# Performance work log

Hardware: AMD Instinct MI355X
Metric: run time of the kernel (lower is better)

Reference implementation:

```python
import jax, jax.numpy as jnp
import numpy as np
import math

B, T, C, H = 2, 2048, 1024, 16
HD = C // H  # head_dim = 64


def setup_inputs() -> dict:
    key = jax.random.key(0)
    ks = jax.random.split(key, 10)
    s = 1.0 / math.sqrt(C)
    x = jax.random.normal(ks[0], (B, T, C), jnp.float32)
    wq = jax.random.normal(ks[1], (C, C), jnp.float32) * s
    wk = jax.random.normal(ks[2], (C, C), jnp.float32) * s
    wv = jax.random.normal(ks[3], (C, C), jnp.float32) * s
    wo = jax.random.normal(ks[4], (C, C), jnp.float32) * s
    bq = jnp.zeros((C,), jnp.float32)
    bk = jnp.zeros((C,), jnp.float32)
    bv = jnp.zeros((C,), jnp.float32)
    bo = jnp.zeros((C,), jnp.float32)
    fractal_dim = jnp.ones((1,), jnp.float32)  # scalar fractal dimension input
    alpha = jnp.asarray(1.5, jnp.float32)
    fractal_alpha_scale = jnp.asarray(0.5, jnp.float32)
    energy_normalizer = jnp.asarray(1.0, jnp.float32)
    return {"x": x, "fractal_dim": fractal_dim, "wq": wq, "bq": bq, "wk": wk,
            "bk": bk, "wv": wv, "bv": bv, "wo": wo, "bo": bo, "alpha": alpha,
            "fractal_alpha_scale": fractal_alpha_scale,
            "energy_normalizer": energy_normalizer}


def reference(x, fractal_dim, wq, bq, wk, bk, wv, bv, wo, bo, alpha,
              fractal_alpha_scale, energy_normalizer):
    b, t, c = x.shape
    # input energy: L2 norm over channels, [b, t, 1]
    input_energy = jnp.linalg.norm(x, axis=-1, keepdims=True)
    adaptive_alpha = alpha + fractal_alpha_scale * (fractal_dim - 1.5)  # [1]

    q = (x @ wq + bq).reshape(b, t, H, HD)
    k = (x @ wk + bk).reshape(b, t, H, HD)
    v = (x @ wv + bv).reshape(b, t, H, HD)

    # per-head FFT along the time axis -> complex64
    q_fft = jnp.fft.fft(q, axis=1)
    k_fft = jnp.fft.fft(k, axis=1)
    v_fft = jnp.fft.fft(v, axis=1)

    freqs = jnp.fft.fftfreq(t).astype(jnp.float32)  # [t]
    phase = adaptive_alpha * jnp.arctan(jnp.log(jnp.abs(freqs) + 1e-10))  # [t]
    # unit-modulus complex spectral filter, broadcast [1, t, 1, 1]
    filt = jax.lax.complex(jnp.cos(phase), jnp.sin(phase))[None, :, None, None]

    qf = q_fft * filt
    kf = k_fft * filt
    vf = v_fft * filt

    # real part of complex matmul Q_f @ K_f^T, computed without complex GEMM:
    # Re(qf kf^T) = qr kr^T - qi ki^T
    inv_sqrt = np.float32(1.0 / math.sqrt(HD))
    logits = (jnp.einsum('bthd,bshd->bhts', qf.real, kf.real)
              - jnp.einsum('bthd,bshd->bhts', qf.imag, kf.imag)) * inv_sqrt
    attn = jax.nn.softmax(logits, axis=-1)  # [b, h, t, s]

    # attn is real, so Re(attn @ vf) = attn @ Re(vf); out_proj has real weights
    # so taking the real part before the projection is exact.
    attended = jnp.einsum('bhts,bshd->bthd', attn, vf.real)
    out = attended.reshape(b, t, c) @ wo + bo

    out_energy = jnp.linalg.norm(out, axis=-1, keepdims=True)
    energy_ratio = input_energy / (out_energy + 1e-8)
    return out * energy_ratio * energy_normalizer
```

## Files before the change

### kernel.cpp

```cpp
#include <hip/hip_runtime.h>
#include <math.h>


typedef _Float16 half8 __attribute__((ext_vector_type(8)));
typedef _Float16 half4 __attribute__((ext_vector_type(4)));
typedef float f32x4 __attribute__((ext_vector_type(4)));
#define MFMA16 __builtin_amdgcn_mfma_f32_16x16x32_f16

#define GLOAD16(g, l) __builtin_amdgcn_global_load_lds( \
    (const __attribute__((address_space(1))) void*)(g), \
    (__attribute__((address_space(3))) void*)(l), 16, 0, 0)

__device__ inline void split2(float v, _Float16& h, _Float16& l) {
    h = (_Float16)v;
    l = (_Float16)((v - (float)h) * 2048.0f);
}
__device__ inline unsigned pack_split(float v) {
    _Float16 h, l;
    split2(v, h, l);
    union { _Float16 f; unsigned short u; } a, b;
    a.f = h; b.f = l;
    return (unsigned)a.u | ((unsigned)b.u << 16);
}
__device__ inline _Float16 lo16(unsigned u) {
    union { unsigned short s; _Float16 f; } x; x.s = (unsigned short)(u & 0xffffu); return x.f;
}
__device__ inline _Float16 hi16(unsigned u) {
    union { unsigned short s; _Float16 f; } x; x.s = (unsigned short)(u >> 16); return x.f;
}
__device__ inline float2 cmul(float2 a, float2 b) {
    return make_float2(a.x * b.x - a.y * b.y, a.x * b.y + a.y * b.x);
}

__device__ inline void write_split(_Float16* dh, _Float16* dl, uint4 u0, uint4 u1) {
    uint4 lo, hi;
    lo.x = __builtin_amdgcn_perm(u0.y, u0.x, 0x05040100u);
    lo.y = __builtin_amdgcn_perm(u0.w, u0.z, 0x05040100u);
    lo.z = __builtin_amdgcn_perm(u1.y, u1.x, 0x05040100u);
    lo.w = __builtin_amdgcn_perm(u1.w, u1.z, 0x05040100u);
    hi.x = __builtin_amdgcn_perm(u0.y, u0.x, 0x07060302u);
    hi.y = __builtin_amdgcn_perm(u0.w, u0.z, 0x07060302u);
    hi.z = __builtin_amdgcn_perm(u1.y, u1.x, 0x07060302u);
    hi.w = __builtin_amdgcn_perm(u1.w, u1.z, 0x07060302u);
    *(uint4*)dh = lo;
    *(uint4*)dl = hi;
}

__global__ __launch_bounds__(256) void k_init_tables(
    float2* __restrict__ tw, float2* __restrict__ filt,
    const float* __restrict__ fd, const float* __restrict__ alpha,
    const float* __restrict__ fas)
{
    int i = blockIdx.x * 256 + threadIdx.x;
    double aa = (double)alpha[0] + (double)fas[0] * ((double)fd[0] - 1.5);
    if (i < 1024) {
        double ang = -2.0 * 3.14159265358979323846 * (double)i / 2048.0;
        double s, c;
        sincos(ang, &s, &c);
        tw[i] = make_float2((float)c, (float)s);
    }
    if (i < 2048) {
        double fr = (i < 1024) ? (double)i / 2048.0 : ((double)i - 2048.0) / 2048.0;
        double ph = aa * atan(log(fabs(fr) + 1e-10));
        double s, c;
        sincos(ph, &s, &c);
        filt[i] = make_float2((float)c, (float)s);
    }
}

__global__ __launch_bounds__(256) void k_prep_wpl3(
    const float* __restrict__ wq, const float* __restrict__ wk,
    const float* __restrict__ wv, _Float16* __restrict__ wpl)
{
    __shared__ float tile[64][65];
    const int z = blockIdx.z;
    const float* W = (z == 0) ? wq : (z == 1) ? wk : wv;
    _Float16* Whi = wpl + (size_t)z * 2097152;
    _Float16* Wlo = Whi + 1048576;
    const int kb = blockIdx.x * 64, cb = blockIdx.y * 64;
    const int t = threadIdx.x, r = t >> 4, c4 = (t & 15) * 4;
#pragma unroll
    for (int i = 0; i < 4; ++i) {
        int row = r + 16 * i;
        float4 v = *(const float4*)&W[(size_t)(kb + row) * 1024 + cb + c4];
        tile[row][c4 + 0] = v.x; tile[row][c4 + 1] = v.y;
        tile[row][c4 + 2] = v.z; tile[row][c4 + 3] = v.w;
    }
    __syncthreads();
#pragma unroll
    for (int h = 0; h < 2; ++h) {
        int idx = t + h * 256;
        int lane = idx & 63, kt2 = (idx >> 6) & 1, ct = idx >> 7;
        int cl = ct * 16 + (lane & 15);
        int kl = kt2 * 32 + ((lane >> 4) * 8);
        half8 hv, lv;
#pragma unroll
        for (int j = 0; j < 8; ++j) {
            _Float16 hh, ll;
            split2(tile[kl + j][cl], hh, ll);
            hv[j] = hh; lv[j] = ll;
        }
        size_t u = ((size_t)((cb >> 4) + ct) * 32 + (kb >> 5) + kt2) * 64 + lane;
        *(half8*)&Whi[u * 8] = hv;
        *(half8*)&Wlo[u * 8] = lv;
    }
}

__global__ __launch_bounds__(256) void k_prep_wpl1(
    const float* __restrict__ W, _Float16* __restrict__ wpl)
{
    __shared__ float tile[64][65];
    _Float16* Whi = wpl;
    _Float16* Wlo = wpl + 1048576;
    const int kb = blockIdx.x * 64, cb = blockIdx.y * 64;
    const int t = threadIdx.x, r = t >> 4, c4 = (t & 15) * 4;
#pragma unroll
    for (int i = 0; i < 4; ++i) {
        int row = r + 16 * i;
        float4 v = *(const float4*)&W[(size_t)(kb + row) * 1024 + cb + c4];
        tile[row][c4 + 0] = v.x; tile[row][c4 + 1] = v.y;
        tile[row][c4 + 2] = v.z; tile[row][c4 + 3] = v.w;
    }
    __syncthreads();
#pragma unroll
    for (int h = 0; h < 2; ++h) {
        int idx = t + h * 256;
        int lane = idx & 63, kt2 = (idx >> 6) & 1, ct = idx >> 7;
        int cl = ct * 16 + (lane & 15);
        int kl = kt2 * 32 + ((lane >> 4) * 8);
        half8 hv, lv;
#pragma unroll
        for (int j = 0; j < 8; ++j) {
            _Float16 hh, ll;
            split2(tile[kl + j][cl], hh, ll);
            hv[j] = hh; lv[j] = ll;
        }
        size_t u = ((size_t)((cb >> 4) + ct) * 32 + (kb >> 5) + kt2) * 64 + lane;
        *(half8*)&Whi[u * 8] = hv;
        *(half8*)&Wlo[u * 8] = lv;
    }
}

__global__ __launch_bounds__(256) void k_prep_xpl(
    const float* __restrict__ x, _Float16* __restrict__ xpl)
{
    __shared__ float tile[64][65];
    _Float16* Xhi = xpl;
    _Float16* Xlo = xpl + 4194304;
    const int nb = blockIdx.x * 64, cb = blockIdx.y * 64;
    const int t = threadIdx.x, r = t >> 4, c4 = (t & 15) * 4;
#pragma unroll
    for (int i = 0; i < 4; ++i) {
        int row = r + 16 * i;
        float4 v = *(const float4*)&x[(size_t)(nb + row) * 1024 + cb + c4];
        tile[row][c4 + 0] = v.x; tile[row][c4 + 1] = v.y;
        tile[row][c4 + 2] = v.z; tile[row][c4 + 3] = v.w;
    }
    __syncthreads();
#pragma unroll
    for (int h = 0; h < 2; ++h) {
        int idx = t + h * 256;
        int lane = idx & 63, ct2 = (idx >> 6) & 1, ntl = (idx >> 7) & 3;
        int nl = ntl * 16 + (lane & 15);
        int cl = ct2 * 32 + ((lane >> 4) * 8);
        half8 hv, lv;
#pragma unroll
        for (int j = 0; j < 8; ++j) {
            _Float16 hh, ll;
            split2(tile[nl][cl + j], hh, ll);
            hv[j] = hh; lv[j] = ll;
        }
        size_t u = ((size_t)((nb >> 4) + ntl) * 32 + (cb >> 5) + ct2) * 64 + lane;
        *(half8*)&Xhi[u * 8] = hv;
        *(half8*)&Xlo[u * 8] = lv;
    }
}

__global__ __launch_bounds__(256) void k_gemm_qkv(
    const _Float16* __restrict__ xpl, const _Float16* __restrict__ wpl,
    const float* __restrict__ bq, const float* __restrict__ bk,
    const float* __restrict__ bv,
    float* __restrict__ qT, float* __restrict__ kT, float* __restrict__ vT)
{
    __shared__ __align__(16) _Float16 Ab[2][8][2][64][8];
    __shared__ __align__(16) _Float16 Bb[2][8][2][64][8];
    const int tid = threadIdx.x;
    const int mat = blockIdx.z;
    const _Float16* Ahi = wpl + (size_t)mat * 2097152;
    const _Float16* Alo = Ahi + 1048576;
    const _Float16* Bhi = xpl;
    const _Float16* Blo = xpl + 4194304;
    const float* bias = (mat == 0) ? bq : (mat == 1) ? bk : bv;
    float* outp       = (mat == 0) ? qT : (mat == 1) ? kT : vT;
    const int m0 = blockIdx.x * 128, n0 = blockIdx.y * 128;
    const int w = tid >> 6, lane = tid & 63, quad = lane >> 4, l15 = lane & 15;
    const int wm = (w & 1) * 4, wn = (w >> 1) * 4;

    const int s0 = 2 * w, s1 = 2 * w + 1;
    const size_t aT0 = (size_t)((m0 >> 4) + s0) * 32;
    const size_t aT1 = aT0 + 32;
    const size_t bT0 = (size_t)((n0 >> 4) + s0) * 32;
    const size_t bT1 = bT0 + 32;
    const int ln8 = lane * 8;

    f32x4 acc1[4][4], acc2[4][4];
    const f32x4 z4 = {0.f, 0.f, 0.f, 0.f};
#pragma unroll
    for (int i = 0; i < 4; ++i)
#pragma unroll
        for (int j = 0; j < 4; ++j) { acc1[i][j] = z4; acc2[i][j] = z4; }

    {
        size_t oA0 = aT0 * 512 + ln8;
        size_t oA1 = aT1 * 512 + ln8;
        size_t oB0 = bT0 * 512 + ln8;
        size_t oB1 = bT1 * 512 + ln8;
        GLOAD16(Ahi + oA0, &Ab[0][s0][0][0][0]);
        GLOAD16(Alo + oA0, &Ab[0][s0][1][0][0]);
        GLOAD16(Ahi + oA1, &Ab[0][s1][0][0][0]);
        GLOAD16(Alo + oA1, &Ab[0][s1][1][0][0]);
        GLOAD16(Bhi + oB0, &Bb[0][s0][0][0][0]);
        GLOAD16(Blo + oB0, &Bb[0][s0][1][0][0]);
        GLOAD16(Bhi + oB1, &Bb[0][s1][0][0][0]);
        GLOAD16(Blo + oB1, &Bb[0][s1][1][0][0]);
    }
    __syncthreads();

    for (int kt = 0; kt < 32; ++kt) {
        const int cur = kt & 1, nxt = cur ^ 1;
        if (kt < 31) {
            int kn = kt + 1;
            size_t oA0 = (aT0 + kn) * 512 + ln8;
            size_t oA1 = (aT1 + kn) * 512 + ln8;
            size_t oB0 = (bT0 + kn) * 512 + ln8;
            size_t oB1 = (bT1 + kn) * 512 + ln8;
            GLOAD16(Ahi + oA0, &Ab[nxt][s0][0][0][0]);
            GLOAD16(Alo + oA0, &Ab[nxt][s0][1][0][0]);
            GLOAD16(Ahi + oA1, &Ab[nxt][s1][0][0][0]);
            GLOAD16(Alo + oA1, &Ab[nxt][s1][1][0][0]);
            GLOAD16(Bhi + oB0, &Bb[nxt][s0][0][0][0]);
            GLOAD16(Blo + oB0, &Bb[nxt][s0][1][0][0]);
            GLOAD16(Bhi + oB1, &Bb[nxt][s1][0][0][0]);
            GLOAD16(Blo + oB1, &Bb[nxt][s1][1][0][0]);
        }
        half8 ah[4], al[4];
#pragma unroll
        for (int mt = 0; mt < 4; ++mt) {
            ah[mt] = *(half8*)&Ab[cur][wm + mt][0][lane][0];
            al[mt] = *(half8*)&Ab[cur][wm + mt][1][lane][0];
        }
#pragma unroll
        for (int nt = 0; nt < 4; ++nt) {
            half8 bh = *(half8*)&Bb[cur][wn + nt][0][lane][0];
            half8 bl = *(half8*)&Bb[cur][wn + nt][1][lane][0];
#pragma unroll
            for (int mt = 0; mt < 4; ++mt) {
                acc1[mt][nt] = MFMA16(ah[mt], bh, acc1[mt][nt], 0, 0, 0);
                acc2[mt][nt] = MFMA16(ah[mt], bl, acc2[mt][nt], 0, 0, 0);
                acc2[mt][nt] = MFMA16(al[mt], bh, acc2[mt][nt], 0, 0, 0);
            }
        }
        __syncthreads();
    }
    const int b_ = n0 >> 11, t0 = n0 & 2047;
#pragma unroll
    for (int mt = 0; mt < 4; ++mt) {
#pragma unroll
        for (int r_ = 0; r_ < 4; ++r_) {
            int m = m0 + (wm + mt) * 16 + quad * 4 + r_;
            float bs = bias[m];
            float* orow = &outp[(size_t)(b_ * 1024 + m) * 2048 + t0];
#pragma unroll
            for (int nt = 0; nt < 4; ++nt) {
                float val = acc1[mt][nt][r_] + acc2[mt][nt][r_] * (1.f / 2048.f) + bs;
                orow[(wn + nt) * 16 + l15] = val;
            }
        }
    }
}

#define SFI(i) ((i) + ((i) >> 4))
__global__ __launch_bounds__(256) void k_fft_filter(
    float* __restrict__ qT, float* __restrict__ kT, float* __restrict__ vT,
    float* __restrict__ qiT, float* __restrict__ kiT,
    const float2* __restrict__ tw, const float2* __restrict__ filt)
{
    __shared__ float2 sf[2176];
    const int bid = blockIdx.x;
    const int mat = bid >> 10;
    const int pair = bid & 1023;
    const int seq0 = pair * 2, seq1 = seq0 + 1;
    float* base = (mat == 0) ? qT : (mat == 1) ? kT : vT;
    float* src0 = base + (size_t)seq0 * 2048;
    float* src1 = base + (size_t)seq1 * 2048;
    const int tid = threadIdx.x;

    for (int i = tid; i < 2048; i += 256) {
        int j = (int)(__brev((unsigned)i) >> 21);
        sf[SFI(j)] = make_float2(src0[i], src1[i]);
    }
    __syncthreads();
#pragma unroll
    for (int st = 1; st <= 9; st += 2) {
        const int h = 1 << (st - 1);
        const int s = 11 - st;
        for (int u = tid; u < 512; u += 256) {
            int m = u & (h - 1);
            int g = u >> (st - 1);
            int bi = g * 4 * h + m;
            float2 a = sf[SFI(bi)], b = sf[SFI(bi + h)];
            float2 c = sf[SFI(bi + 2 * h)], d = sf[SFI(bi + 3 * h)];
            float2 W  = tw[m << s];
            float2 W2 = tw[m << (s - 1)];
            float2 wb = cmul(W, b), wd = cmul(W, d);
            float2 a1 = make_float2(a.x + wb.x, a.y + wb.y);
            float2 b1 = make_float2(a.x - wb.x, a.y - wb.y);
            float2 c1 = make_float2(c.x + wd.x, c.y + wd.y);
            float2 d1 = make_float2(c.x - wd.x, c.y - wd.y);
            float2 w2c = cmul(W2, c1);
            float2 w2d = cmul(W2, d1);
            float2 w3d = make_float2(w2d.y, -w2d.x);
            sf[SFI(bi)]         = make_float2(a1.x + w2c.x, a1.y + w2c.y);
            sf[SFI(bi + 2 * h)] = make_float2(a1.x - w2c.x, a1.y - w2c.y);
            sf[SFI(bi + h)]     = make_float2(b1.x + w3d.x, b1.y + w3d.y);
            sf[SFI(bi + 3 * h)] = make_float2(b1.x - w3d.x, b1.y - w3d.y);
        }
        __syncthreads();
    }
    for (int u = tid; u < 1024; u += 256) {
        float2 w = tw[u];
        float2 a = sf[SFI(u)], b = sf[SFI(u + 1024)];
        float2 wb = cmul(w, b);
        sf[SFI(u)]        = make_float2(a.x + wb.x, a.y + wb.y);
        sf[SFI(u + 1024)] = make_float2(a.x - wb.x, a.y - wb.y);
    }
    __syncthreads();

    unsigned* dr0 = (unsigned*)src0;
    unsigned* dr1 = (unsigned*)src1;
    unsigned* di0 = (mat == 0) ? (unsigned*)(qiT + (size_t)seq0 * 2048)
                               : (unsigned*)(kiT + (size_t)seq0 * 2048);
    unsigned* di1 = (mat == 0) ? (unsigned*)(qiT + (size_t)seq1 * 2048)
                               : (unsigned*)(kiT + (size_t)seq1 * 2048);
    for (int i = tid; i < 2048; i += 256) {
        float2 z  = sf[SFI(i)];
        float2 zm = sf[SFI((2048 - i) & 2047)];
        float Are = 0.5f * (z.x + zm.x), Aim = 0.5f * (z.y - zm.y);
        float Bre = 0.5f * (z.y + zm.y), Bim = 0.5f * (zm.x - z.x);
        float2 f = filt[i];
        float re0 = Are * f.x - Aim * f.y, im0 = Are * f.y + Aim * f.x;
        float re1 = Bre * f.x - Bim * f.y, im1 = Bre * f.y + Bim * f.x;
        if (mat == 0) {
            dr0[i] = pack_split(0.125f * re0); di0[i] = pack_split(0.125f * im0);
            dr1[i] = pack_split(0.125f * re1); di1[i] = pack_split(0.125f * im1);
        } else if (mat == 1) {
            dr0[i] = pack_split(re0); di0[i] = pack_split(-im0);
            dr1[i] = pack_split(re1); di1[i] = pack_split(-im1);
        } else {
            dr0[i] = pack_split(re0);
            dr1[i] = pack_split(re1);
        }
    }
}

__global__ __launch_bounds__(512, 2) void k_flash(
    const unsigned* __restrict__ qpk, const unsigned* __restrict__ qipk,
    const unsigned* __restrict__ kpk, const unsigned* __restrict__ kipk,
    const unsigned* __restrict__ vpk, _Float16* __restrict__ attpl)
{
    __shared__ __align__(16) _Float16 Kbuf[2][4][4][2][64][8];
    __shared__ __align__(16) _Float16 Vbuf[2][2][4][2][64][8];

    const int tid = threadIdx.x;
    const int w = tid >> 6, lane = tid & 63;
    const int quad = lane >> 4, l15 = lane & 15;
    const int p = blockIdx.x;
    const int bh = (p & 7) * 4 + (p >> 6);
    const int tb = (p >> 3) & 7;
    const size_t bc = (size_t)bh * 64;
    const int tw0 = tb * 256 + w * 16;

    half8 aqh[2][4], aql[2][4];
#pragma unroll
    for (int rg = 0; rg < 2; ++rg) {
#pragma unroll
        for (int kc = 0; kc < 4; ++kc) {
#pragma unroll
            for (int j = 0; j < 8; ++j) {
                int d = kc * 32 + quad * 8 + j;
                int t = tw0 + rg * 128 + l15;
                unsigned u = (d < 64) ? qpk[(bc + d) * 2048 + t]
                                      : qipk[(bc + d - 64) * 2048 + t];
                aqh[rg][kc][j] = lo16(u);
                aql[rg][kc][j] = hi16(u);
            }
        }
    }

    f32x4 O1[2][4], O2[2][4];
    const f32x4 zero4 = {0.f, 0.f, 0.f, 0.f};
#pragma unroll
    for (int rg = 0; rg < 2; ++rg)
#pragma unroll
        for (int nt = 0; nt < 4; ++nt) { O1[rg][nt] = zero4; O2[rg][nt] = zero4; }
    float m_[2] = {-3e38f, -3e38f};
    float l_[2] = {0.f, 0.f};

    const int sK = tid & 63;
    const int dc0 = tid >> 6;
    const int stK = sK >> 4;
    const int kcK0 = dc0 >> 2;
    const int laneK = (sK & 15) + ((dc0 & 3) << 4);
    const unsigned* kre = &kpk[(bc + dc0 * 8) * 2048 + sK];
    const unsigned* kim = &kipk[(bc + dc0 * 8) * 2048 + sK];
    const int sc2V = tid >> 8;
    const int ntV = (tid >> 6) & 3, laneV = tid & 63;
    const int dV = ntV * 16 + (laneV & 15);
    const int s0V = sc2V * 32 + (laneV >> 4) * 4;
    const unsigned* vbase = &vpk[(bc + dV) * 2048 + s0V];

    unsigned ka0, ka1, ka2, ka3, ka4, ka5, ka6, ka7;
    unsigned kb0, kb1, kb2, kb3, kb4, kb5, kb6, kb7;
    uint4 va0, va1;
    ka0 = kre[0 * 2048]; ka1 = kre[1 * 2048];
    ka2 = kre[2 * 2048]; ka3 = kre[3 * 2048];
    ka4 = kre[4 * 2048]; ka5 = kre[5 * 2048];
    ka6 = kre[6 * 2048]; ka7 = kre[7 * 2048];
    kb0 = kim[0 * 2048]; kb1 = kim[1 * 2048];
    kb2 = kim[2 * 2048]; kb3 = kim[3 * 2048];
    kb4 = kim[4 * 2048]; kb5 = kim[5 * 2048];
    kb6 = kim[6 * 2048]; kb7 = kim[7 * 2048];
    va0 = *(const uint4*)vbase;
    va1 = *(const uint4*)(vbase + 16);
    write_split(&Kbuf[0][stK][kcK0][0][laneK][0], &Kbuf[0][stK][kcK0][1][laneK][0],
                make_uint4(ka0, ka1, ka2, ka3), make_uint4(ka4, ka5, ka6, ka7));
    write_split(&Kbuf[0][stK][kcK0 + 2][0][laneK][0], &Kbuf[0][stK][kcK0 + 2][1][laneK][0],
                make_uint4(kb0, kb1, kb2, kb3), make_uint4(kb4, kb5, kb6, kb7));
    write_split(&Vbuf[0][sc2V][ntV][0][laneV][0], &Vbuf[0][sc2V][ntV][1][laneV][0],
                va0, va1);
    kre += 64; kim += 64; vbase += 64;
    ka0 = kre[0 * 2048]; ka1 = kre[1 * 2048];
    ka2 = kre[2 * 2048]; ka3 = kre[3 * 2048];
    ka4 = kre[4 * 2048]; ka5 = kre[5 * 2048];
    ka6 = kre[6 * 2048]; ka7 = kre[7 * 2048];
    kb0 = kim[0 * 2048]; kb1 = kim[1 * 2048];
    kb2 = kim[2 * 2048]; kb3 = kim[3 * 2048];
    kb4 = kim[4 * 2048]; kb5 = kim[5 * 2048];
    kb6 = kim[6 * 2048]; kb7 = kim[7 * 2048];
    va0 = *(const uint4*)vbase;
    va1 = *(const uint4*)(vbase + 16);
    __syncthreads();

    for (int it = 0; it < 32; ++it) {
        const int cur = it & 1, nxt = cur ^ 1;
        if (it < 31) {
            write_split(&Kbuf[nxt][stK][kcK0][0][laneK][0],
                        &Kbuf[nxt][stK][kcK0][1][laneK][0],
                        make_uint4(ka0, ka1, ka2, ka3), make_uint4(ka4, ka5, ka6, ka7));
            write_split(&Kbuf[nxt][stK][kcK0 + 2][0][laneK][0],
                        &Kbuf[nxt][stK][kcK0 + 2][1][laneK][0],
                        make_uint4(kb0, kb1, kb2, kb3), make_uint4(kb4, kb5, kb6, kb7));
            write_split(&Vbuf[nxt][sc2V][ntV][0][laneV][0],
                        &Vbuf[nxt][sc2V][ntV][1][laneV][0], va0, va1);
        }
        if (it < 30) {
            kre += 64; kim += 64; vbase += 64;
            ka0 = kre[0 * 2048]; ka1 = kre[1 * 2048];
            ka2 = kre[2 * 2048]; ka3 = kre[3 * 2048];
            ka4 = kre[4 * 2048]; ka5 = kre[5 * 2048];
            ka6 = kre[6 * 2048]; ka7 = kre[7 * 2048];
            kb0 = kim[0 * 2048]; kb1 = kim[1 * 2048];
            kb2 = kim[2 * 2048]; kb3 = kim[3 * 2048];
            kb4 = kim[4 * 2048]; kb5 = kim[5 * 2048];
            kb6 = kim[6 * 2048]; kb7 = kim[7 * 2048];
            va0 = *(const uint4*)vbase;
            va1 = *(const uint4*)(vbase + 16);
        }

        f32x4 S1[2][4], S2[2][4];
#pragma unroll
        for (int rg = 0; rg < 2; ++rg)
#pragma unroll
            for (int st = 0; st < 4; ++st) { S1[rg][st] = zero4; S2[rg][st] = zero4; }
        __builtin_amdgcn_s_setprio(1);
#pragma unroll
        for (int st = 0; st < 4; ++st) {
#pragma unroll
            for (int kc = 0; kc < 4; ++kc) {
                half8 khf = *(half8*)&Kbuf[cur][st][kc][0][lane][0];
                half8 klf = *(half8*)&Kbuf[cur][st][kc][1][lane][0];
#pragma unroll
                for (int rg = 0; rg < 2; ++rg) {
                    S1[rg][st] = MFMA16(khf, aqh[rg][kc], S1[rg][st], 0, 0, 0);
                    S2[rg][st] = MFMA16(klf, aqh[rg][kc], S2[rg][st], 0, 0, 0);
                    S2[rg][st] = MFMA16(khf, aql[rg][kc], S2[rg][st], 0, 0, 0);
                }
            }
        }
        __builtin_amdgcn_s_setprio(0);

        half8 pb[2][2];
#pragma unroll
        for (int rg = 0; rg < 2; ++rg) {
#pragma unroll
            for (int st = 0; st < 4; ++st)
                S1[rg][st] = S1[rg][st] + S2[rg][st] * (1.f / 2048.f);
            float mt = -3e38f;
#pragma unroll
            for (int st = 0; st < 4; ++st)
#pragma unroll
                for (int r = 0; r < 4; ++r)
                    mt = fmaxf(mt, S1[rg][st][r]);
            mt = fmaxf(mt, __shfl_xor(mt, 16));
            mt = fmaxf(mt, __shfl_xor(mt, 32));
            if (!__all(mt <= m_[rg] + 8.f)) {
                float mn2 = fmaxf(m_[rg], mt);
                float al = __expf(m_[rg] - mn2);
                m_[rg] = mn2;
                l_[rg] *= al;
#pragma unroll
                for (int nt = 0; nt < 4; ++nt) { O1[rg][nt] *= al; O2[rg][nt] *= al; }
            }
            float mn = m_[rg];
            float rs = 0.f;
            _Float16 ph[4][4];
#pragma unroll
            for (int st = 0; st < 4; ++st)
#pragma unroll
                for (int r = 0; r < 4; ++r) {
                    float pe = __expf(S1[rg][st][r] - mn);
                    rs += pe;
                    ph[st][r] = (_Float16)pe;
                }
            rs += __shfl_xor(rs, 16);
            rs += __shfl_xor(rs, 32);
            l_[rg] += rs;
#pragma unroll
            for (int sc2 = 0; sc2 < 2; ++sc2) {
                half8 t8;
                t8[0] = ph[2 * sc2][0];     t8[1] = ph[2 * sc2][1];
                t8[2] = ph[2 * sc2][2];     t8[3] = ph[2 * sc2][3];
                t8[4] = ph[2 * sc2 + 1][0]; t8[5] = ph[2 * sc2 + 1][1];
                t8[6] = ph[2 * sc2 + 1][2]; t8[7] = ph[2 * sc2 + 1][3];
                pb[rg][sc2] = t8;
            }
        }

        __builtin_amdgcn_s_setprio(1);
#pragma unroll
        for (int sc2 = 0; sc2 < 2; ++sc2) {
#pragma unroll
            for (int nt = 0; nt < 4; ++nt) {
                half8 vh = *(half8*)&Vbuf[cur][sc2][nt][0][lane][0];
                half8 vl = *(half8*)&Vbuf[cur][sc2][nt][1][lane][0];
                O1[0][nt] = MFMA16(vh, pb[0][sc2], O1[0][nt], 0, 0, 0);
                O2[0][nt] = MFMA16(vl, pb[0][sc2], O2[0][nt], 0, 0, 0);
                O1[1][nt] = MFMA16(vh, pb[1][sc2], O1[1][nt], 0, 0, 0);
                O2[1][nt] = MFMA16(vl, pb[1][sc2], O2[1][nt], 0, 0, 0);
            }
        }
        __builtin_amdgcn_s_setprio(0);

        __syncthreads();
    }

    const int b = bh >> 4, h = bh & 15;
#pragma unroll
    for (int rg = 0; rg < 2; ++rg) {
        float inv = 1.0f / l_[rg];
        int mrow = b * 2048 + tw0 + rg * 128 + l15;
        size_t mt32 = (size_t)(mrow >> 4) * 32;
#pragma unroll
        for (int nt = 0; nt < 4; ++nt) {
            size_t u = (mt32 + h * 2 + (nt >> 1)) * 512
                     + (size_t)(l15 + 16 * ((nt * 2 + (quad >> 1)) & 3)) * 8
                     + (quad & 1) * 4;
            half4 hv, lv;
#pragma unroll
            for (int r = 0; r < 4; ++r) {
                float val = (O1[rg][nt][r] + O2[rg][nt][r] * (1.f / 2048.f)) * inv;
                _Float16 hh, ll;
                split2(val, hh, ll);
                hv[r] = hh; lv[r] = ll;
            }
            *(half4*)&attpl[u] = hv;
            *(half4*)&attpl[4194304 + u] = lv;
        }
    }
}

__global__ __launch_bounds__(256) void k_gemm_out(
    const _Float16* __restrict__ attpl, const _Float16* __restrict__ wopl,
    const float* __restrict__ bo, float* __restrict__ out)
{
    __shared__ __align__(16) _Float16 Ab[2][8][2][64][8];
    __shared__ __align__(16) _Float16 Bb[2][8][2][64][8];
    const int tid = threadIdx.x;
    const _Float16* Ahi = attpl;
    const _Float16* Alo = attpl + 4194304;
    const _Float16* Bhi = wopl;
    const _Float16* Blo = wopl + 1048576;
    const int m0 = blockIdx.x * 128, n0 = blockIdx.y * 128;
    const int w = tid >> 6, lane = tid & 63, quad = lane >> 4, l15 = lane & 15;
    const int wm = (w & 1) * 4, wn = (w >> 1) * 4;

    const int s0 = 2 * w, s1 = 2 * w + 1;
    const size_t aT0 = (size_t)((m0 >> 4) + s0) * 32;
    const size_t aT1 = aT0 + 32;
    const size_t bT0 = (size_t)((n0 >> 4) + s0) * 32;
    const size_t bT1 = bT0 + 32;
    const int ln8 = lane * 8;

    f32x4 acc1[4][4], acc2[4][4];
    const f32x4 z4 = {0.f, 0.f, 0.f, 0.f};
#pragma unroll
    for (int i = 0; i < 4; ++i)
#pragma unroll
        for (int j = 0; j < 4; ++j) { acc1[i][j] = z4; acc2[i][j] = z4; }

    {
        size_t oA0 = aT0 * 512 + ln8;
        size_t oA1 = aT1 * 512 + ln8;
        size_t oB0 = bT0 * 512 + ln8;
        size_t oB1 = bT1 * 512 + ln8;
        GLOAD16(Ahi + oA0, &Ab[0][s0][0][0][0]);
        GLOAD16(Alo + oA0, &Ab[0][s0][1][0][0]);
        GLOAD16(Ahi + oA1, &Ab[0][s1][0][0][0]);
        GLOAD16(Alo + oA1, &Ab[0][s1][1][0][0]);
        GLOAD16(Bhi + oB0, &Bb[0][s0][0][0][0]);
        GLOAD16(Blo + oB0, &Bb[0][s0][1][0][0]);
        GLOAD16(Bhi + oB1, &Bb[0][s1][0][0][0]);
        GLOAD16(Blo + oB1, &Bb[0][s1][1][0][0]);
    }
    __syncthreads();

    for (int kt = 0; kt < 32; ++kt) {
        const int cur = kt & 1, nxt = cur ^ 1;
        if (kt < 31) {
            int kn = kt + 1;
            size_t oA0 = (aT0 + kn) * 512 + ln8;
            size_t oA1 = (aT1 + kn) * 512 + ln8;
            size_t oB0 = (bT0 + kn) * 512 + ln8;
            size_t oB1 = (bT1 + kn) * 512 + ln8;
            GLOAD16(Ahi + oA0, &Ab[nxt][s0][0][0][0]);
            GLOAD16(Alo + oA0, &Ab[nxt][s0][1][0][0]);
            GLOAD16(Ahi + oA1, &Ab[nxt][s1][0][0][0]);
            GLOAD16(Alo + oA1, &Ab[nxt][s1][1][0][0]);
            GLOAD16(Bhi + oB0, &Bb[nxt][s0][0][0][0]);
            GLOAD16(Blo + oB0, &Bb[nxt][s0][1][0][0]);
            GLOAD16(Bhi + oB1, &Bb[nxt][s1][0][0][0]);
            GLOAD16(Blo + oB1, &Bb[nxt][s1][1][0][0]);
        }
        half8 ah[4], al[4];
#pragma unroll
        for (int mt = 0; mt < 4; ++mt) {
            ah[mt] = *(half8*)&Ab[cur][wm + mt][0][lane][0];
            al[mt] = *(half8*)&Ab[cur][wm + mt][1][lane][0];
        }
#pragma unroll
        for (int nt = 0; nt < 4; ++nt) {
            half8 bh = *(half8*)&Bb[cur][wn + nt][0][lane][0];
            half8 bl = *(half8*)&Bb[cur][wn + nt][1][lane][0];
#pragma unroll
            for (int mt = 0; mt < 4; ++mt) {
                acc1[mt][nt] = MFMA16(ah[mt], bh, acc1[mt][nt], 0, 0, 0);
                acc2[mt][nt] = MFMA16(ah[mt], bl, acc2[mt][nt], 0, 0, 0);
                acc2[mt][nt] = MFMA16(al[mt], bh, acc2[mt][nt], 0, 0, 0);
            }
        }
        __syncthreads();
    }
#pragma unroll
    for (int mt = 0; mt < 4; ++mt) {
#pragma unroll
        for (int r_ = 0; r_ < 4; ++r_) {
            int m = m0 + (wm + mt) * 16 + quad * 4 + r_;
            float* orow = &out[(size_t)m * 1024 + n0];
#pragma unroll
            for (int nt = 0; nt < 4; ++nt) {
                int n = (wn + nt) * 16 + l15;
                float val = acc1[mt][nt][r_] + acc2[mt][nt][r_] * (1.f / 2048.f)
                          + bo[n0 + n];
                orow[n] = val;
            }
        }
    }
}

__global__ __launch_bounds__(256) void k_norm(
    const float* __restrict__ x, float* __restrict__ out,
    const float* __restrict__ en)
{
    const int row = blockIdx.x;
    const int tid = threadIdx.x;
    const float* xr = x + (size_t)row * 1024;
    float* orow = out + (size_t)row * 1024;
    float4 xv = *(const float4*)&xr[tid * 4];
    float4 ov = *(const float4*)&orow[tid * 4];
    float ssx = xv.x * xv.x + xv.y * xv.y + xv.z * xv.z + xv.w * xv.w;
    float sso = ov.x * ov.x + ov.y * ov.y + ov.z * ov.z + ov.w * ov.w;
#pragma unroll
    for (int m = 1; m <= 32; m <<= 1) {
        ssx += __shfl_xor(ssx, m, 64);
        sso += __shfl_xor(sso, m, 64);
    }
    __shared__ float rx[4], ro[4];
    const int wid = tid >> 6;
    if ((tid & 63) == 0) { rx[wid] = ssx; ro[wid] = sso; }
    __syncthreads();
    float tsx = rx[0] + rx[1] + rx[2] + rx[3];
    float tso = ro[0] + ro[1] + ro[2] + ro[3];
    float scale = sqrtf(tsx) / (sqrtf(tso) + 1e-8f) * en[0];
    ov.x *= scale; ov.y *= scale; ov.z *= scale; ov.w *= scale;
    *(float4*)&orow[tid * 4] = ov;
}

extern "C" void kernel_launch(void* const* d_in, const int* in_sizes, int n_in,
                              void* d_out, int out_size, void* d_ws, size_t ws_size,
                              hipStream_t stream)
{
    const float* x     = (const float*)d_in[0];
    const float* fd    = (const float*)d_in[1];
    const float* wq    = (const float*)d_in[2];
    const float* bq    = (const float*)d_in[3];
    const float* wk    = (const float*)d_in[4];
    const float* bk    = (const float*)d_in[5];
    const float* wv    = (const float*)d_in[6];
    const float* bv    = (const float*)d_in[7];
    const float* wo    = (const float*)d_in[8];
    const float* bo    = (const float*)d_in[9];
    const float* alpha = (const float*)d_in[10];
    const float* fas   = (const float*)d_in[11];
    const float* en    = (const float*)d_in[12];
    float* out = (float*)d_out;
    float* ws  = (float*)d_ws;

    float* qT  = ws;
    float* kT  = ws + (size_t)1 * 4194304;
    float* vT  = ws + (size_t)2 * 4194304;
    float* qiT = ws + (size_t)3 * 4194304;
    float* kiT = ws + (size_t)4 * 4194304;
    float* att = ws + (size_t)5 * 4194304;
    float2* tw   = (float2*)(ws + (size_t)6 * 4194304);
    float2* filt = (float2*)(ws + (size_t)6 * 4194304 + 2048);

    _Float16* wpl   = (_Float16*)qiT;
    _Float16* xpl   = (_Float16*)att;
    _Float16* attpl = (_Float16*)att;
    _Float16* wopl  = (_Float16*)qT;

    k_init_tables<<<8, 256, 0, stream>>>(tw, filt, fd, alpha, fas);
    k_prep_wpl3<<<dim3(16, 16, 3), 256, 0, stream>>>(wq, wk, wv, wpl);
    k_prep_xpl<<<dim3(64, 16), 256, 0, stream>>>(x, xpl);
    k_gemm_qkv<<<dim3(8, 32, 3), 256, 0, stream>>>(xpl, wpl, bq, bk, bv,
                                                   qT, kT, vT);
    k_fft_filter<<<3072, 256, 0, stream>>>(qT, kT, vT, qiT, kiT, tw, filt);
    k_flash<<<256, 512, 0, stream>>>((const unsigned*)qT, (const unsigned*)qiT,
                                     (const unsigned*)kT, (const unsigned*)kiT,
                                     (const unsigned*)vT, attpl);
    k_prep_wpl1<<<dim3(16, 16), 256, 0, stream>>>(wo, wopl);
    k_gemm_out<<<dim3(32, 8), 256, 0, stream>>>(attpl, wopl, bo, out);
    k_norm<<<4096, 256, 0, stream>>>(x, out, en);
}
```

Before: 424.8 us.

## Halve flash-attention block and KV tile sizes to double grid size

The flash attention kernel now runs 512 blocks of 256 threads, each covering 128 query rows instead of 256, and streams K/V in 32-key tiles over 64 iterations instead of 64-key tiles over 32. The loader index mapping and LDS buffers are reshaped to match. This gives 512 blocks across the GPU's compute units instead of 256, for better occupancy and load balance, and uses smaller shared-memory buffers. In exchange, K/V are reloaded by twice as many blocks and each block runs twice as many barrier-synchronised iterations with less MFMA work per barrier.

Measured after the change: 454.2 us. 6.9% more time.

```diff
diff --git a/kernel.cpp b/kernel.cpp
--- a/kernel.cpp
+++ b/kernel.cpp
@@ -363,22 +363,22 @@
     }
 }
 
-__global__ __launch_bounds__(512, 2) void k_flash(
+__global__ __launch_bounds__(256, 2) void k_flash(
     const unsigned* __restrict__ qpk, const unsigned* __restrict__ qipk,
     const unsigned* __restrict__ kpk, const unsigned* __restrict__ kipk,
     const unsigned* __restrict__ vpk, _Float16* __restrict__ attpl)
 {
-    __shared__ __align__(16) _Float16 Kbuf[2][4][4][2][64][8];
-    __shared__ __align__(16) _Float16 Vbuf[2][2][4][2][64][8];
+    __shared__ __align__(16) _Float16 Kbuf[2][2][4][2][64][8];
+    __shared__ __align__(16) _Float16 Vbuf[2][4][2][64][8];
 
     const int tid = threadIdx.x;
     const int w = tid >> 6, lane = tid & 63;
     const int quad = lane >> 4, l15 = lane & 15;
     const int p = blockIdx.x;
-    const int bh = (p & 7) * 4 + (p >> 6);
-    const int tb = (p >> 3) & 7;
+    const int bh = (p & 7) * 4 + (p >> 7);
+    const int tb = (p >> 3) & 15;
     const size_t bc = (size_t)bh * 64;
-    const int tw0 = tb * 256 + w * 16;
+    const int tw0 = tb * 128 + w * 16;
 
     half8 aqh[2][4], aql[2][4];
 #pragma unroll
@@ -388,7 +388,7 @@
 #pragma unroll
             for (int j = 0; j < 8; ++j) {
                 int d = kc * 32 + quad * 8 + j;
-                int t = tw0 + rg * 128 + l15;
+                int t = tw0 + rg * 64 + l15;
                 unsigned u = (d < 64) ? qpk[(bc + d) * 2048 + t]
                                       : qipk[(bc + d - 64) * 2048 + t];
                 aqh[rg][kc][j] = lo16(u);
@@ -406,18 +406,17 @@
     float m_[2] = {-3e38f, -3e38f};
     float l_[2] = {0.f, 0.f};
 
-    const int sK = tid & 63;
-    const int dc0 = tid >> 6;
+    const int sK = tid & 31;
+    const int dgK = tid >> 5;
     const int stK = sK >> 4;
-    const int kcK0 = dc0 >> 2;
-    const int laneK = (sK & 15) + ((dc0 & 3) << 4);
-    const unsigned* kre = &kpk[(bc + dc0 * 8) * 2048 + sK];
-    const unsigned* kim = &kipk[(bc + dc0 * 8) * 2048 + sK];
-    const int sc2V = tid >> 8;
-    const int ntV = (tid >> 6) & 3, laneV = tid & 63;
+    const int kcK0 = dgK >> 2;
+    const int laneK = (sK & 15) + ((dgK & 3) << 4);
+    const unsigned* kre = &kpk[(bc + dgK * 8) * 2048 + sK];
+    const unsigned* kim = &kipk[(bc + dgK * 8) * 2048 + sK];
+    const int ntV = tid >> 6, laneV = tid & 63;
     const int dV = ntV * 16 + (laneV & 15);
-    const int s0V = sc2V * 32 + (laneV >> 4) * 4;
-    const unsigned* vbase = &vpk[(bc + dV) * 2048 + s0V];
+    const int qV4 = (laneV >> 4) * 4;
+    const unsigned* vbase = &vpk[(bc + dV) * 2048 + qV4];
 
     unsigned ka0, ka1, ka2, ka3, ka4, ka5, ka6, ka7;
     unsigned kb0, kb1, kb2, kb3, kb4, kb5, kb6, kb7;
@@ -436,9 +435,8 @@
                 make_uint4(ka0, ka1, ka2, ka3), make_uint4(ka4, ka5, ka6, ka7));
     write_split(&Kbuf[0][stK][kcK0 + 2][0][laneK][0], &Kbuf[0][stK][kcK0 + 2][1][laneK][0],
                 make_uint4(kb0, kb1, kb2, kb3), make_uint4(kb4, kb5, kb6, kb7));
-    write_split(&Vbuf[0][sc2V][ntV][0][laneV][0], &Vbuf[0][sc2V][ntV][1][laneV][0],
-                va0, va1);
-    kre += 64; kim += 64; vbase += 64;
+    write_split(&Vbuf[0][ntV][0][laneV][0], &Vbuf[0][ntV][1][laneV][0], va0, va1);
+    kre += 32; kim += 32; vbase += 32;
     ka0 = kre[0 * 2048]; ka1 = kre[1 * 2048];
     ka2 = kre[2 * 2048]; ka3 = kre[3 * 2048];
     ka4 = kre[4 * 2048]; ka5 = kre[5 * 2048];
@@ -451,20 +449,20 @@
     va1 = *(const uint4*)(vbase + 16);
     __syncthreads();
 
-    for (int it = 0; it < 32; ++it) {
+    for (int it = 0; it < 64; ++it) {
         const int cur = it & 1, nxt = cur ^ 1;
-        if (it < 31) {
+        if (it < 63) {
             write_split(&Kbuf[nxt][stK][kcK0][0][laneK][0],
                         &Kbuf[nxt][stK][kcK0][1][laneK][0],
                         make_uint4(ka0, ka1, ka2, ka3), make_uint4(ka4, ka5, ka6, ka7));
             write_split(&Kbuf[nxt][stK][kcK0 + 2][0][laneK][0],
                         &Kbuf[nxt][stK][kcK0 + 2][1][laneK][0],
                         make_uint4(kb0, kb1, kb2, kb3), make_uint4(kb4, kb5, kb6, kb7));
-            write_split(&Vbuf[nxt][sc2V][ntV][0][laneV][0],
-                        &Vbuf[nxt][sc2V][ntV][1][laneV][0], va0, va1);
-        }
-        if (it < 30) {
-            kre += 64; kim += 64; vbase += 64;
+            write_split(&Vbuf[nxt][ntV][0][laneV][0],
+                        &Vbuf[nxt][ntV][1][laneV][0], va0, va1);
+        }
+        if (it < 62) {
+            kre += 32; kim += 32; vbase += 32;
             ka0 = kre[0 * 2048]; ka1 = kre[1 * 2048];
             ka2 = kre[2 * 2048]; ka3 = kre[3 * 2048];
             ka4 = kre[4 * 2048]; ka5 = kre[5 * 2048];
@@ -477,14 +475,14 @@
             va1 = *(const uint4*)(vbase + 16);
         }
 
-        f32x4 S1[2][4], S2[2][4];
+        f32x4 S1[2][2], S2[2][2];
 #pragma unroll
         for (int rg = 0; rg < 2; ++rg)
 #pragma unroll
-            for (int st = 0; st < 4; ++st) { S1[rg][st] = zero4; S2[rg][st] = zero4; }
+            for (int st = 0; st < 2; ++st) { S1[rg][st] = zero4; S2[rg][st] = zero4; }
         __builtin_amdgcn_s_setprio(1);
 #pragma unroll
-        for (int st = 0; st < 4; ++st) {
+        for (int st = 0; st < 2; ++st) {
 #pragma unroll
             for (int kc = 0; kc < 4; ++kc) {
                 half8 khf = *(half8*)&Kbuf[cur][st][kc][0][lane][0];
@@ -499,15 +497,15 @@
         }
         __builtin_amdgcn_s_setprio(0);
 
-        half8 pb[2][2];
+        half8 pb[2];
 #pragma unroll
         for (int rg = 0; rg < 2; ++rg) {
 #pragma unroll
-            for (int st = 0; st < 4; ++st)
+            for (int st = 0; st < 2; ++st)
                 S1[rg][st] = S1[rg][st] + S2[rg][st] * (1.f / 2048.f);
             float mt = -3e38f;
 #pragma unroll
-            for (int st = 0; st < 4; ++st)
+            for (int st = 0; st < 2; ++st)
 #pragma unroll
                 for (int r = 0; r < 4; ++r)
                     mt = fmaxf(mt, S1[rg][st][r]);
@@ -523,9 +521,9 @@
             }
             float mn = m_[rg];
             float rs = 0.f;
-            _Float16 ph[4][4];
-#pragma unroll
-            for (int st = 0; st < 4; ++st)
+            _Float16 ph[2][4];
+#pragma unroll
+            for (int st = 0; st < 2; ++st)
 #pragma unroll
                 for (int r = 0; r < 4; ++r) {
                     float pe = __expf(S1[rg][st][r] - mn);
@@ -535,29 +533,23 @@
             rs += __shfl_xor(rs, 16);
             rs += __shfl_xor(rs, 32);
             l_[rg] += rs;
-#pragma unroll
-            for (int sc2 = 0; sc2 < 2; ++sc2) {
-                half8 t8;
-                t8[0] = ph[2 * sc2][0];     t8[1] = ph[2 * sc2][1];
-                t8[2] = ph[2 * sc2][2];     t8[3] = ph[2 * sc2][3];
-                t8[4] = ph[2 * sc2 + 1][0]; t8[5] = ph[2 * sc2 + 1][1];
-                t8[6] = ph[2 * sc2 + 1][2]; t8[7] = ph[2 * sc2 + 1][3];
-                pb[rg][sc2] = t8;
-            }
+            half8 t8;
+            t8[0] = ph[0][0]; t8[1] = ph[0][1];
+            t8[2] = ph[0][2]; t8[3] = ph[0][3];
+            t8[4] = ph[1][0]; t8[5] = ph[1][1];
+            t8[6] = ph[1][2]; t8[7] = ph[1][3];
+            pb[rg] = t8;
         }
 
         __builtin_amdgcn_s_setprio(1);
 #pragma unroll
-        for (int sc2 = 0; sc2 < 2; ++sc2) {
-#pragma unroll
-            for (int nt = 0; nt < 4; ++nt) {
-                half8 vh = *(half8*)&Vbuf[cur][sc2][nt][0][lane][0];
-                half8 vl = *(half8*)&Vbuf[cur][sc2][nt][1][lane][0];
-                O1[0][nt] = MFMA16(vh, pb[0][sc2], O1[0][nt], 0, 0, 0);
-                O2[0][nt] = MFMA16(vl, pb[0][sc2], O2[0][nt], 0, 0, 0);
-                O1[1][nt] = MFMA16(vh, pb[1][sc2], O1[1][nt], 0, 0, 0);
-                O2[1][nt] = MFMA16(vl, pb[1][sc2], O2[1][nt], 0, 0, 0);
-            }
+        for (int nt = 0; nt < 4; ++nt) {
+            half8 vh = *(half8*)&Vbuf[cur][nt][0][lane][0];
+            half8 vl = *(half8*)&Vbuf[cur][nt][1][lane][0];
+            O1[0][nt] = MFMA16(vh, pb[0], O1[0][nt], 0, 0, 0);
+            O2[0][nt] = MFMA16(vl, pb[0], O2[0][nt], 0, 0, 0);
+            O1[1][nt] = MFMA16(vh, pb[1], O1[1][nt], 0, 0, 0);
+            O2[1][nt] = MFMA16(vl, pb[1], O2[1][nt], 0, 0, 0);
         }
         __builtin_amdgcn_s_setprio(0);
 
@@ -568,7 +560,7 @@
 #pragma unroll
     for (int rg = 0; rg < 2; ++rg) {
         float inv = 1.0f / l_[rg];
-        int mrow = b * 2048 + tw0 + rg * 128 + l15;
+        int mrow = b * 2048 + tw0 + rg * 64 + l15;
         size_t mt32 = (size_t)(mrow >> 4) * 32;
 #pragma unroll
         for (int nt = 0; nt < 4; ++nt) {
@@ -755,7 +747,7 @@
     k_gemm_qkv<<<dim3(8, 32, 3), 256, 0, stream>>>(xpl, wpl, bq, bk, bv,
                                                    qT, kT, vT);
     k_fft_filter<<<3072, 256, 0, stream>>>(qT, kT, vT, qiT, kiT, tw, filt);
-    k_flash<<<256, 512, 0, stream>>>((const unsigned*)qT, (const unsigned*)qiT,
+    k_flash<<<512, 256, 0, stream>>>((const unsigned*)qT, (const unsigned*)qiT,
                                      (const unsigned*)kT, (const unsigned*)kiT,
                                      (const unsigned*)vT, attpl);
     k_prep_wpl1<<<dim3(16, 16), 256, 0, stream>>>(wo, wopl);
```
